# Kernel tuning notes

Measured on AMD Instinct MI355X. Metric: run time of the kernel, lower is better.

Reference implementation:

```python
import jax, jax.numpy as jnp
import numpy as np

BLOCK = 64          # block_size
R = 64              # number of OFT blocks (r)
N_ELEM = BLOCK * (BLOCK - 1) // 2  # 2016 upper-triangular elements per block
TOKENS = 8192       # batch*seq tokens
IN_FEATURES = R * BLOCK  # 4096
NUM_TERMS = 5       # num_cayley_neumann_terms

_ROWS, _COLS = jnp.triu_indices(BLOCK, k=1)


def _skew_symmetric(vec):
    # vec: [r, n_elements] -> [r, BLOCK, BLOCK] skew-symmetric
    m = jnp.zeros((vec.shape[0], BLOCK, BLOCK), dtype=vec.dtype)
    m = m.at[:, _ROWS, _COLS].set(vec)
    return m - jnp.swapaxes(m, -2, -1)


def _cayley_neumann(weight):
    # Neumann approximation of Cayley transform:
    # R = I + 2*Q + 2*Q^2 + ... + 2*Q^(NUM_TERMS-1)
    Q = _skew_symmetric(weight)                      # [r, B, B]
    eye = jnp.eye(BLOCK, dtype=weight.dtype)
    rot = eye[None, :, :] + 2.0 * Q
    Q_pow = Q
    for _ in range(2, NUM_TERMS):
        Q_pow = jnp.einsum('rij,rjk->rik', Q_pow, Q)
        rot = rot + 2.0 * Q_pow
    return rot                                        # [r, B, B]


def setup_inputs() -> dict:
    key = jax.random.key(0)
    k1, k2 = jax.random.split(key)
    x = jax.random.normal(k1, (TOKENS, IN_FEATURES), dtype=jnp.float32)
    # OFT weights start near zero (rotation ~ identity); small scale keeps
    # the Neumann series well-conditioned.
    weight = jax.random.normal(k2, (R, N_ELEM), dtype=jnp.float32) * 0.02
    return {"x": x, "weight": weight}


def reference(x, weight):
    rot = _cayley_neumann(weight)                      # [r, B, B]
    xr = x.reshape(x.shape[0], R, BLOCK)               # [n, r, B]
    out = jnp.einsum('nrk,rkc->nrc', xr, rot)          # block-diag rotation
    return out.reshape(x.shape)
```

## Files before the change

### kernel.cpp

```cpp
#include <hip/hip_runtime.h>


#define NELEM 2016

__device__ __forceinline__ int triu_off(int i) {
    return i * 63 - (i * (i - 1)) / 2;
}

__global__ __launch_bounds__(1024) void oft_rot_kernel(const float* __restrict__ w,
                                                       float* __restrict__ rot) {
    __shared__ float Q[64][64];
    __shared__ float P[2][64][64];

    const int r   = blockIdx.x;
    const float* __restrict__ wr = w + r * NELEM;
    const int tid = threadIdx.x;
    const int i   = tid >> 4;
    const int j0  = (tid & 15) << 2;

    float racc[4];
#pragma unroll
    for (int t = 0; t < 4; ++t) {
        const int j = j0 + t;
        float v;
        if (i < j)      v =  wr[triu_off(i) + (j - i - 1)];
        else if (i > j) v = -wr[triu_off(j) + (i - j - 1)];
        else            v = 0.f;
        Q[i][j]    = v;
        P[0][i][j] = v;
        racc[t] = (i == j ? 1.f : 0.f) + 2.f * v;
    }
    __syncthreads();

    int cur = 0;
#pragma unroll
    for (int p = 2; p < 5; ++p) {
        float a0 = 0.f, a1 = 0.f, a2 = 0.f, a3 = 0.f;
#pragma unroll
        for (int k = 0; k < 64; ++k) {
            const float  pv = P[cur][i][k];
            const float4 qv = *(const float4*)&Q[k][j0];
            a0 = fmaf(pv, qv.x, a0);
            a1 = fmaf(pv, qv.y, a1);
            a2 = fmaf(pv, qv.z, a2);
            a3 = fmaf(pv, qv.w, a3);
        }
        P[cur ^ 1][i][j0 + 0] = a0;
        P[cur ^ 1][i][j0 + 1] = a1;
        P[cur ^ 1][i][j0 + 2] = a2;
        P[cur ^ 1][i][j0 + 3] = a3;
        racc[0] += 2.f * a0;
        racc[1] += 2.f * a1;
        racc[2] += 2.f * a2;
        racc[3] += 2.f * a3;
        __syncthreads();
        cur ^= 1;
    }

    float4 o = make_float4(racc[0], racc[1], racc[2], racc[3]);
    *(float4*)&rot[(size_t)r * 4096 + i * 64 + j0] = o;
}

__global__ __launch_bounds__(256, 3) void oft_apply_kernel(const float* __restrict__ x,
                                                           const float* __restrict__ rot,
                                                           float* __restrict__ out) {
    const int lane = threadIdx.x & 63;
    const int wv   = threadIdx.x >> 6;
    const int r    = blockIdx.x;
    const int n    = blockIdx.y * 256 + wv * 64 + lane;

    const float* __restrict__ xp = x + (size_t)n * 4096 + r * 64;
    const float* __restrict__ rt = rot + (size_t)r * 4096;

    float xr[64];
#pragma unroll
    for (int q = 0; q < 16; ++q) {
        const float4 v = *(const float4*)(xp + q * 4);
        xr[q * 4 + 0] = v.x;
        xr[q * 4 + 1] = v.y;
        xr[q * 4 + 2] = v.z;
        xr[q * 4 + 3] = v.w;
    }

    float* __restrict__ op = out + (size_t)n * 4096 + r * 64;

    for (int cc = 0; cc < 64; cc += 8) {
        float acc[8] = {0.f, 0.f, 0.f, 0.f, 0.f, 0.f, 0.f, 0.f};
#pragma unroll
        for (int k = 0; k < 64; ++k) {
            const float xv = xr[k];
#pragma unroll
            for (int j = 0; j < 8; ++j)
                acc[j] = fmaf(rt[k * 64 + cc + j], xv, acc[j]);
        }
        float4 o0 = make_float4(acc[0], acc[1], acc[2], acc[3]);
        float4 o1 = make_float4(acc[4], acc[5], acc[6], acc[7]);
        *(float4*)(op + cc)     = o0;
        *(float4*)(op + cc + 4) = o1;
    }
}

extern "C" void kernel_launch(void* const* d_in, const int* in_sizes, int n_in,
                              void* d_out, int out_size, void* d_ws, size_t ws_size,
                              hipStream_t stream) {
    const float* x = (const float*)d_in[0];
    const float* w = (const float*)d_in[1];
    float* out = (float*)d_out;
    float* rot = (float*)d_ws;

    oft_rot_kernel<<<64, 1024, 0, stream>>>(w, rot);
    oft_apply_kernel<<<dim3(64, 32), 256, 0, stream>>>(x, rot, out);
}
```

Measured before the change: 309.3 us.

## Stage rotation and token tiles in LDS for apply kernel; split rot kernel rows

The apply kernel now stages each block's 64x64 rotation matrix and a 128-token x tile in shared memory. Each thread computes an 8-token by 4-column register tile, reusing every loaded rotation row across 8 tokens. This replaces the old per-thread scheme, where each thread held 64 inputs in registers and read the rotation matrix from global memory repeatedly, and it gives coalesced float4 output stores. The rotation kernel is split across 4 row tiles per block with 256 threads each to spread the small setup work over more CUs, at the cost of recomputing Q in each tile. The extra LDS footprint (about 49KB per block) may limit occupancy.

Measured after the change: 250.0 us. -19.2%, faster.

```diff
diff --git a/kernel.cpp b/kernel.cpp
--- a/kernel.cpp
+++ b/kernel.cpp
@@ -7,28 +7,40 @@
     return i * 63 - (i * (i - 1)) / 2;
 }
 
-__global__ __launch_bounds__(1024) void oft_rot_kernel(const float* __restrict__ w,
-                                                       float* __restrict__ rot) {
+__device__ __forceinline__ float skew_val(const float* __restrict__ wr, int i, int j) {
+    if (i < j) return  wr[triu_off(i) + (j - i - 1)];
+    if (i > j) return -wr[triu_off(j) + (i - j - 1)];
+    return 0.f;
+}
+
+__global__ __launch_bounds__(256) void oft_rot_kernel(const float* __restrict__ w,
+                                                      float* __restrict__ rot) {
     __shared__ float Q[64][64];
-    __shared__ float P[2][64][64];
+    __shared__ float Pl[2][16][65];
 
-    const int r   = blockIdx.x;
+    const int r    = blockIdx.x;
+    const int tile = blockIdx.y;
     const float* __restrict__ wr = w + r * NELEM;
     const int tid = threadIdx.x;
-    const int i   = tid >> 4;
+    const int il  = tid >> 4;
     const int j0  = (tid & 15) << 2;
+    const int gi  = tile * 16 + il;
+
+#pragma unroll
+    for (int m = 0; m < 4; ++m) {
+        const int i = il + 16 * m;
+#pragma unroll
+        for (int t = 0; t < 4; ++t)
+            Q[i][j0 + t] = skew_val(wr, i, j0 + t);
+    }
+    __syncthreads();
 
     float racc[4];
 #pragma unroll
     for (int t = 0; t < 4; ++t) {
-        const int j = j0 + t;
-        float v;
-        if (i < j)      v =  wr[triu_off(i) + (j - i - 1)];
-        else if (i > j) v = -wr[triu_off(j) + (i - j - 1)];
-        else            v = 0.f;
-        Q[i][j]    = v;
-        P[0][i][j] = v;
-        racc[t] = (i == j ? 1.f : 0.f) + 2.f * v;
+        const float qv = Q[gi][j0 + t];
+        Pl[0][il][j0 + t] = qv;
+        racc[t] = (gi == j0 + t ? 1.f : 0.f) + 2.f * qv;
     }
     __syncthreads();
 
@@ -36,19 +48,19 @@
 #pragma unroll
     for (int p = 2; p < 5; ++p) {
         float a0 = 0.f, a1 = 0.f, a2 = 0.f, a3 = 0.f;
-#pragma unroll
+#pragma unroll 8
         for (int k = 0; k < 64; ++k) {
-            const float  pv = P[cur][i][k];
+            const float  pv = Pl[cur][il][k];
             const float4 qv = *(const float4*)&Q[k][j0];
             a0 = fmaf(pv, qv.x, a0);
             a1 = fmaf(pv, qv.y, a1);
             a2 = fmaf(pv, qv.z, a2);
             a3 = fmaf(pv, qv.w, a3);
         }
-        P[cur ^ 1][i][j0 + 0] = a0;
-        P[cur ^ 1][i][j0 + 1] = a1;
-        P[cur ^ 1][i][j0 + 2] = a2;
-        P[cur ^ 1][i][j0 + 3] = a3;
+        Pl[cur ^ 1][il][j0 + 0] = a0;
+        Pl[cur ^ 1][il][j0 + 1] = a1;
+        Pl[cur ^ 1][il][j0 + 2] = a2;
+        Pl[cur ^ 1][il][j0 + 3] = a3;
         racc[0] += 2.f * a0;
         racc[1] += 2.f * a1;
         racc[2] += 2.f * a2;
@@ -57,46 +69,69 @@
         cur ^= 1;
     }
 
-    float4 o = make_float4(racc[0], racc[1], racc[2], racc[3]);
-    *(float4*)&rot[(size_t)r * 4096 + i * 64 + j0] = o;
+    *(float4*)&rot[(size_t)r * 4096 + gi * 64 + j0] =
+        make_float4(racc[0], racc[1], racc[2], racc[3]);
 }
 
 __global__ __launch_bounds__(256, 3) void oft_apply_kernel(const float* __restrict__ x,
                                                            const float* __restrict__ rot,
                                                            float* __restrict__ out) {
-    const int lane = threadIdx.x & 63;
-    const int wv   = threadIdx.x >> 6;
-    const int r    = blockIdx.x;
-    const int n    = blockIdx.y * 256 + wv * 64 + lane;
+    __shared__ float rotS[64][64];
+    __shared__ float xs[128][65];
 
-    const float* __restrict__ xp = x + (size_t)n * 4096 + r * 64;
-    const float* __restrict__ rt = rot + (size_t)r * 4096;
+    const int r   = blockIdx.x;
+    const int tok0 = blockIdx.y * 128;
+    const int tid = threadIdx.x;
 
-    float xr[64];
+    {
+        const float4* __restrict__ src = (const float4*)(rot + (size_t)r * 4096);
+        float4* dst = (float4*)&rotS[0][0];
 #pragma unroll
-    for (int q = 0; q < 16; ++q) {
-        const float4 v = *(const float4*)(xp + q * 4);
-        xr[q * 4 + 0] = v.x;
-        xr[q * 4 + 1] = v.y;
-        xr[q * 4 + 2] = v.z;
-        xr[q * 4 + 3] = v.w;
+        for (int p = 0; p < 4; ++p)
+            dst[p * 256 + tid] = src[p * 256 + tid];
+    }
+#pragma unroll
+    for (int p = 0; p < 8; ++p) {
+        const int f   = p * 256 + tid;
+        const int row = f >> 4;
+        const int c   = (f & 15) << 2;
+        const float4 v = *(const float4*)(x + (size_t)(tok0 + row) * 4096 + r * 64 + c);
+        xs[row][c + 0] = v.x;
+        xs[row][c + 1] = v.y;
+        xs[row][c + 2] = v.z;
+        xs[row][c + 3] = v.w;
+    }
+    __syncthreads();
+
+    const int cq = tid & 15;
+    const int tq = tid >> 4;
+    const int c0 = cq << 2;
+    const float* __restrict__ xbase = &xs[tq * 8][0];
+
+    float acc[8][4];
+#pragma unroll
+    for (int m = 0; m < 8; ++m)
+#pragma unroll
+        for (int t = 0; t < 4; ++t) acc[m][t] = 0.f;
+
+#pragma unroll 8
+    for (int k = 0; k < 64; ++k) {
+        const float4 rv = *(const float4*)&rotS[k][c0];
+#pragma unroll
+        for (int m = 0; m < 8; ++m) {
+            const float xv = xbase[m * 65 + k];
+            acc[m][0] = fmaf(xv, rv.x, acc[m][0]);
+            acc[m][1] = fmaf(xv, rv.y, acc[m][1]);
+            acc[m][2] = fmaf(xv, rv.z, acc[m][2]);
+            acc[m][3] = fmaf(xv, rv.w, acc[m][3]);
+        }
     }
 
-    float* __restrict__ op = out + (size_t)n * 4096 + r * 64;
-
-    for (int cc = 0; cc < 64; cc += 8) {
-        float acc[8] = {0.f, 0.f, 0.f, 0.f, 0.f, 0.f, 0.f, 0.f};
 #pragma unroll
-        for (int k = 0; k < 64; ++k) {
-            const float xv = xr[k];
-#pragma unroll
-            for (int j = 0; j < 8; ++j)
-                acc[j] = fmaf(rt[k * 64 + cc + j], xv, acc[j]);
-        }
-        float4 o0 = make_float4(acc[0], acc[1], acc[2], acc[3]);
-        float4 o1 = make_float4(acc[4], acc[5], acc[6], acc[7]);
-        *(float4*)(op + cc)     = o0;
-        *(float4*)(op + cc + 4) = o1;
+    for (int m = 0; m < 8; ++m) {
+        const int n = tok0 + tq * 8 + m;
+        *(float4*)(out + (size_t)n * 4096 + r * 64 + c0) =
+            make_float4(acc[m][0], acc[m][1], acc[m][2], acc[m][3]);
     }
 }
 
@@ -108,6 +143,6 @@
     float* out = (float*)d_out;
     float* rot = (float*)d_ws;
 
-    oft_rot_kernel<<<64, 1024, 0, stream>>>(w, rot);
-    oft_apply_kernel<<<dim3(64, 32), 256, 0, stream>>>(x, rot, out);
+    oft_rot_kernel<<<dim3(64, 4), 256, 0, stream>>>(w, rot);
+    oft_apply_kernel<<<dim3(64, 64), 256, 0, stream>>>(x, rot, out);
 }
```
